# Performance work log

Measured on AMD Instinct MI355X. Metric: run time of the kernel, lower is better.

Reference implementation:

```python
import jax, jax.numpy as jnp
import numpy as np

B, S, D = 4, 16, 512          # batch, seq, attention_dim
V, T = 32000, 18              # vocab_size, tree_depth
INNER = V - 1                 # internal nodes of Huffman tree


def setup_inputs() -> dict:
    key = jax.random.key(0)
    k_att, k_w, k_idx, k_bit = jax.random.split(key, 4)
    att = jax.random.normal(k_att, (B, S, D), dtype=jnp.float32)
    weight = jax.random.normal(k_w, (INNER, D), dtype=jnp.float32) * 0.02
    path_index = jax.random.randint(k_idx, (V * T,), 0, INNER, dtype=jnp.int64)
    # left/right branch bits: sign=+1,bias=0 -> p ; sign=-1,bias=1 -> 1-p
    bits = jax.random.randint(k_bit, (V * T,), 0, 2).astype(jnp.float32)
    path_sign = 1.0 - 2.0 * bits
    path_bias = bits
    return {
        "att": att,
        "weight": weight,
        "path_index": path_index,
        "path_sign": path_sign,
        "path_bias": path_bias,
        "vocab_size": V,
        "tree_depth": T,
    }


def reference(att, weight, path_index, path_sign, path_bias, vocab_size, tree_depth):
    # h: sigmoid of linear projection onto internal-node vectors  [B,S,INNER]
    h = jax.nn.sigmoid(jnp.einsum("bsd,nd->bsn", att, weight))
    # gather per-(token,depth) internal-node probs, flip via sign/bias
    g = jnp.take(h, path_index, axis=-1) * path_sign + path_bias  # [B,S,V*T]
    Hm = g.reshape(att.shape[0], -1, vocab_size, tree_depth)      # [B,S,V,T]
    return jnp.sum(jnp.log(Hm), axis=-1)                          # [B,S,V]
```

## Files before the change

kernel.cpp:

```cpp
#include <hip/hip_runtime.h>

#define BS    64
#define DDIM  512
#define NV    32000
#define TD    18
#define INNER 31999

typedef __attribute__((ext_vector_type(8))) short short8;
typedef __attribute__((ext_vector_type(4))) float floatx4;

__device__ __forceinline__ float bf16_to_f32(unsigned short u) {
    union { unsigned int i; float f; } v; v.i = ((unsigned int)u) << 16; return v.f;
}
__device__ __forceinline__ unsigned short f32_to_bf16(float f) {
    union { float f; unsigned int i; } v; v.f = f;
    unsigned int r = v.i + 0x7FFFu + ((v.i >> 16) & 1u);
    return (unsigned short)(r >> 16);
}

#define IDXB 2250
__global__ __launch_bounds__(256) void prep(
    const int* __restrict__ idx,
    const unsigned int* __restrict__ signbits,
    unsigned short* __restrict__ idx2,
    const float4* __restrict__ att,
    ushort4* __restrict__ attb)
{
    const int b = blockIdx.x;
    if (b < IDXB) {
        const unsigned int* w = (const unsigned int*)idx;
        bool i64 = true;
#pragma unroll
        for (int j = 1; j < 16; j += 2) i64 &= (w[j] == 0u);
        int o = b * 256 + threadIdx.x;
        int val = i64 ? idx[2 * o] : idx[o];
        idx2[o] = (unsigned short)((val << 1) | (int)(signbits[o] >> 31));
    } else {
        int i = (b - IDXB) * 256 + threadIdx.x;
        float4 a = att[i];
        ushort4 r;
        r.x = f32_to_bf16(a.x); r.y = f32_to_bf16(a.y);
        r.z = f32_to_bf16(a.z); r.w = f32_to_bf16(a.w);
        attb[i] = r;
    }
}

__global__ __launch_bounds__(256) void gemm_logsig(
    const unsigned short* __restrict__ attb,
    const float* __restrict__ weight,
    unsigned int* __restrict__ pairsT)
{
    const int lane = threadIdx.x & 63;
    const int wave = threadIdx.x >> 6;
    const int nb   = blockIdx.x * 64 + wave * 16;
    const int l15  = lane & 15;
    const int quad = lane >> 4;

    floatx4 acc[4];
#pragma unroll
    for (int i = 0; i < 4; ++i) acc[i] = (floatx4){0.f, 0.f, 0.f, 0.f};

    int brow = nb + l15;
    if (brow > INNER - 1) brow = INNER - 1;
    const float*          bbase = weight + (size_t)brow * DDIM + quad * 8;
    const unsigned short* abase = attb + l15 * DDIM + quad * 8;

#pragma unroll 4
    for (int k0 = 0; k0 < DDIM; k0 += 32) {
        float4 b0 = *(const float4*)(bbase + k0);
        float4 b1 = *(const float4*)(bbase + k0 + 4);
        short8 bfrag;
        bfrag[0] = (short)f32_to_bf16(b0.x); bfrag[1] = (short)f32_to_bf16(b0.y);
        bfrag[2] = (short)f32_to_bf16(b0.z); bfrag[3] = (short)f32_to_bf16(b0.w);
        bfrag[4] = (short)f32_to_bf16(b1.x); bfrag[5] = (short)f32_to_bf16(b1.y);
        bfrag[6] = (short)f32_to_bf16(b1.z); bfrag[7] = (short)f32_to_bf16(b1.w);
#pragma unroll
        for (int mt = 0; mt < 4; ++mt) {
            short8 afrag = *(const short8*)(abase + mt * 16 * DDIM + k0);
            acc[mt] = __builtin_amdgcn_mfma_f32_16x16x32_bf16(afrag, bfrag, acc[mt], 0, 0, 0);
        }
    }

    const int n = nb + l15;
    if (n < INNER) {
        unsigned int* dst = pairsT + ((size_t)n << 6) + quad * 4;
#pragma unroll
        for (int mt = 0; mt < 4; ++mt) {
            unsigned int wds[4];
#pragma unroll
            for (int r = 0; r < 4; ++r) {
                float x = acc[mt][r];
                float lp = -(fmaxf(-x, 0.f) + __logf(1.f + __expf(-fabsf(x))));
                float lm = lp - x;
                wds[r] = (unsigned int)f32_to_bf16(lp)
                       | ((unsigned int)f32_to_bf16(lm) << 16);
            }
            uint4 wv; wv.x = wds[0]; wv.y = wds[1]; wv.z = wds[2]; wv.w = wds[3];
            *(uint4*)(dst + mt * 16) = wv;
        }
    }
}

__global__ __launch_bounds__(256) void gather_bs(
    const unsigned int* __restrict__ pairsT,
    const unsigned short* __restrict__ idx2,
    float* __restrict__ out)
{
    __shared__ float tile[32][65];
    const int lane  = threadIdx.x & 63;
    const int wave  = threadIdx.x >> 6;
    const int vbase = blockIdx.x * 32;

#pragma unroll
    for (int i = 0; i < 8; ++i) {
        const int vloc = wave * 8 + i;
        const unsigned short* col = idx2 + (size_t)(vbase + vloc) * TD;
        float s0 = 0.f, s1 = 0.f;
#pragma unroll
        for (int t = 0; t < TD; t += 2) {
            unsigned int e0 = col[t];
            unsigned int e1 = col[t + 1];
            unsigned int p0 = pairsT[((size_t)(e0 >> 1) << 6) + lane];
            unsigned int p1 = pairsT[((size_t)(e1 >> 1) << 6) + lane];
            unsigned short h0 = (e0 & 1u) ? (unsigned short)(p0 >> 16)
                                          : (unsigned short)(p0 & 0xFFFFu);
            unsigned short h1 = (e1 & 1u) ? (unsigned short)(p1 >> 16)
                                          : (unsigned short)(p1 & 0xFFFFu);
            s0 += bf16_to_f32(h0);
            s1 += bf16_to_f32(h1);
        }
        tile[vloc][lane] = s0 + s1;
    }
    __syncthreads();

    const int bs  = threadIdx.x >> 2;
    const int seg = threadIdx.x & 3;
    float4 r0, r1;
    r0.x = tile[seg * 8 + 0][bs]; r0.y = tile[seg * 8 + 1][bs];
    r0.z = tile[seg * 8 + 2][bs]; r0.w = tile[seg * 8 + 3][bs];
    r1.x = tile[seg * 8 + 4][bs]; r1.y = tile[seg * 8 + 5][bs];
    r1.z = tile[seg * 8 + 6][bs]; r1.w = tile[seg * 8 + 7][bs];
    float4* dst = (float4*)(out + (size_t)bs * NV + vbase + seg * 8);
    dst[0] = r0; dst[1] = r1;
}

extern "C" void kernel_launch(void* const* d_in, const int* in_sizes, int n_in,
                              void* d_out, int out_size, void* d_ws, size_t ws_size,
                              hipStream_t stream)
{
    const float*        att    = (const float*)d_in[0];
    const float*        weight = (const float*)d_in[1];
    const int*          pidx   = (const int*)d_in[2];
    const unsigned int* psign  = (const unsigned int*)d_in[3];
    float* out = (float*)d_out;

    char* ws = (char*)d_ws;
    unsigned int*   pairsT = (unsigned int*)ws;
    unsigned short* idx2   = (unsigned short*)(ws + 8192000);
    ushort4*        attb   = (ushort4*)       (ws + 9344000);

    prep<<<IDXB + 32, 256, 0, stream>>>(pidx, psign, idx2, (const float4*)att, attb);
    gemm_logsig<<<500, 256, 0, stream>>>((const unsigned short*)attb, weight, pairsT);
    gather_bs<<<1000, 256, 0, stream>>>(pairsT, idx2, out);
}
```

Baseline: 138.5 us.

## Stage weight tiles via async global-to-LDS loads and fuse index prep into gather

The GEMM kernel now streams the fp32 weight tile into a double-buffered, XOR-swizzled LDS region with global_load_lds, so the next K-chunk loads while MFMAs run on the current one. Index/sign packing moves out of the prep kernel into the gather kernel, which decodes its 576 path entries into LDS per block. This drops the idx2 round trip through global memory and shrinks prep to the attention conversion. The cost is 64 KB of LDS per GEMM block, which limits occupancy, plus extra barriers and redundant int64 detection in every gather block.

```diff
diff --git a/kernel.cpp b/kernel.cpp
--- a/kernel.cpp
+++ b/kernel.cpp
@@ -17,32 +17,21 @@
     unsigned int r = v.i + 0x7FFFu + ((v.i >> 16) & 1u);
     return (unsigned short)(r >> 16);
 }
+__device__ __forceinline__ void gload16(const void* g, void* l) {
+    __builtin_amdgcn_global_load_lds(
+        (const __attribute__((address_space(1))) unsigned int*)g,
+        (__attribute__((address_space(3))) unsigned int*)l, 16, 0, 0);
+}
 
-#define IDXB 2250
-__global__ __launch_bounds__(256) void prep(
-    const int* __restrict__ idx,
-    const unsigned int* __restrict__ signbits,
-    unsigned short* __restrict__ idx2,
-    const float4* __restrict__ att,
-    ushort4* __restrict__ attb)
+__global__ __launch_bounds__(256) void prep_att(
+    const float4* __restrict__ att, ushort4* __restrict__ attb)
 {
-    const int b = blockIdx.x;
-    if (b < IDXB) {
-        const unsigned int* w = (const unsigned int*)idx;
-        bool i64 = true;
-#pragma unroll
-        for (int j = 1; j < 16; j += 2) i64 &= (w[j] == 0u);
-        int o = b * 256 + threadIdx.x;
-        int val = i64 ? idx[2 * o] : idx[o];
-        idx2[o] = (unsigned short)((val << 1) | (int)(signbits[o] >> 31));
-    } else {
-        int i = (b - IDXB) * 256 + threadIdx.x;
-        float4 a = att[i];
-        ushort4 r;
-        r.x = f32_to_bf16(a.x); r.y = f32_to_bf16(a.y);
-        r.z = f32_to_bf16(a.z); r.w = f32_to_bf16(a.w);
-        attb[i] = r;
-    }
+    int i = blockIdx.x * 256 + threadIdx.x;
+    float4 a = att[i];
+    ushort4 r;
+    r.x = f32_to_bf16(a.x); r.y = f32_to_bf16(a.y);
+    r.z = f32_to_bf16(a.z); r.w = f32_to_bf16(a.w);
+    attb[i] = r;
 }
 
 __global__ __launch_bounds__(256) void gemm_logsig(
@@ -50,50 +39,79 @@
     const float* __restrict__ weight,
     unsigned int* __restrict__ pairsT)
 {
-    const int lane = threadIdx.x & 63;
-    const int wave = threadIdx.x >> 6;
-    const int nb   = blockIdx.x * 64 + wave * 16;
+    __shared__ __align__(16) char ldsb[2][32768];
+
+    const int tid  = threadIdx.x;
+    const int lane = tid & 63;
+    const int wave = tid >> 6;
     const int l15  = lane & 15;
     const int quad = lane >> 4;
+    const int B0   = blockIdx.x * 64;
+
+    const int r    = wave * 16 + l15;
+    const int swz  = (r & 7) << 4;
 
     floatx4 acc[4];
 #pragma unroll
     for (int i = 0; i < 4; ++i) acc[i] = (floatx4){0.f, 0.f, 0.f, 0.f};
 
-    int brow = nb + l15;
-    if (brow > INNER - 1) brow = INNER - 1;
-    const float*          bbase = weight + (size_t)brow * DDIM + quad * 8;
+    auto STAGE = [&](int buf, int c) {
+#pragma unroll
+        for (int it = 0; it < 8; ++it) {
+            int p    = it * 256 + tid;
+            int row  = p >> 5;
+            int cb   = (p & 31) << 4;
+            int gcb  = cb ^ ((row & 7) << 4);
+            int grow = B0 + row;
+            if (grow > INNER - 1) grow = INNER - 1;
+            gload16((const char*)weight + (size_t)grow * (DDIM * 4) + c * 512 + gcb,
+                    &ldsb[buf][row * 512 + cb]);
+        }
+    };
+
+    STAGE(0, 0);
+    __syncthreads();
+
     const unsigned short* abase = attb + l15 * DDIM + quad * 8;
-
-#pragma unroll 4
-    for (int k0 = 0; k0 < DDIM; k0 += 32) {
-        float4 b0 = *(const float4*)(bbase + k0);
-        float4 b1 = *(const float4*)(bbase + k0 + 4);
-        short8 bfrag;
-        bfrag[0] = (short)f32_to_bf16(b0.x); bfrag[1] = (short)f32_to_bf16(b0.y);
-        bfrag[2] = (short)f32_to_bf16(b0.z); bfrag[3] = (short)f32_to_bf16(b0.w);
-        bfrag[4] = (short)f32_to_bf16(b1.x); bfrag[5] = (short)f32_to_bf16(b1.y);
-        bfrag[6] = (short)f32_to_bf16(b1.z); bfrag[7] = (short)f32_to_bf16(b1.w);
+    int buf = 0;
 #pragma unroll
-        for (int mt = 0; mt < 4; ++mt) {
-            short8 afrag = *(const short8*)(abase + mt * 16 * DDIM + k0);
-            acc[mt] = __builtin_amdgcn_mfma_f32_16x16x32_bf16(afrag, bfrag, acc[mt], 0, 0, 0);
+    for (int c = 0; c < 4; ++c) {
+        if (c < 3) STAGE(buf ^ 1, c + 1);
+        const char* bb = &ldsb[buf][r * 512];
+#pragma unroll
+        for (int kl = 0; kl < 4; ++kl) {
+            int cb0 = kl * 128 + quad * 32;
+            float4 b0 = *(const float4*)(bb + ((cb0)      ^ swz));
+            float4 b1 = *(const float4*)(bb + ((cb0 + 16) ^ swz));
+            short8 bfrag;
+            bfrag[0] = (short)f32_to_bf16(b0.x); bfrag[1] = (short)f32_to_bf16(b0.y);
+            bfrag[2] = (short)f32_to_bf16(b0.z); bfrag[3] = (short)f32_to_bf16(b0.w);
+            bfrag[4] = (short)f32_to_bf16(b1.x); bfrag[5] = (short)f32_to_bf16(b1.y);
+            bfrag[6] = (short)f32_to_bf16(b1.z); bfrag[7] = (short)f32_to_bf16(b1.w);
+            const int k0 = c * 128 + kl * 32;
+#pragma unroll
+            for (int mt = 0; mt < 4; ++mt) {
+                short8 afrag = *(const short8*)(abase + mt * 16 * DDIM + k0);
+                acc[mt] = __builtin_amdgcn_mfma_f32_16x16x32_bf16(afrag, bfrag, acc[mt], 0, 0, 0);
+            }
         }
+        __syncthreads();
+        buf ^= 1;
     }
 
-    const int n = nb + l15;
+    const int n = B0 + wave * 16 + l15;
     if (n < INNER) {
         unsigned int* dst = pairsT + ((size_t)n << 6) + quad * 4;
 #pragma unroll
         for (int mt = 0; mt < 4; ++mt) {
             unsigned int wds[4];
 #pragma unroll
-            for (int r = 0; r < 4; ++r) {
-                float x = acc[mt][r];
+            for (int rr = 0; rr < 4; ++rr) {
+                float x = acc[mt][rr];
                 float lp = -(fmaxf(-x, 0.f) + __logf(1.f + __expf(-fabsf(x))));
                 float lm = lp - x;
-                wds[r] = (unsigned int)f32_to_bf16(lp)
-                       | ((unsigned int)f32_to_bf16(lm) << 16);
+                wds[rr] = (unsigned int)f32_to_bf16(lp)
+                        | ((unsigned int)f32_to_bf16(lm) << 16);
             }
             uint4 wv; wv.x = wds[0]; wv.y = wds[1]; wv.z = wds[2]; wv.w = wds[3];
             *(uint4*)(dst + mt * 16) = wv;
@@ -103,18 +121,33 @@
 
 __global__ __launch_bounds__(256) void gather_bs(
     const unsigned int* __restrict__ pairsT,
-    const unsigned short* __restrict__ idx2,
+    const int* __restrict__ idx,
+    const unsigned int* __restrict__ signbits,
     float* __restrict__ out)
 {
+    __shared__ unsigned int eLDS[576];
     __shared__ float tile[32][65];
-    const int lane  = threadIdx.x & 63;
-    const int wave  = threadIdx.x >> 6;
+    const int tid   = threadIdx.x;
+    const int lane  = tid & 63;
+    const int wave  = tid >> 6;
     const int vbase = blockIdx.x * 32;
+
+    const unsigned int* w = (const unsigned int*)idx;
+    bool i64 = true;
+#pragma unroll
+    for (int j = 1; j < 16; j += 2) i64 &= (w[j] == 0u);
+
+    for (int q = tid; q < 576; q += 256) {
+        int g = vbase * TD + q;
+        int val = i64 ? idx[2 * g] : idx[g];
+        eLDS[q] = ((unsigned int)val << 1) | (signbits[g] >> 31);
+    }
+    __syncthreads();
 
 #pragma unroll
     for (int i = 0; i < 8; ++i) {
         const int vloc = wave * 8 + i;
-        const unsigned short* col = idx2 + (size_t)(vbase + vloc) * TD;
+        const unsigned int* col = eLDS + vloc * TD;
         float s0 = 0.f, s1 = 0.f;
 #pragma unroll
         for (int t = 0; t < TD; t += 2) {
@@ -155,11 +188,10 @@
     float* out = (float*)d_out;
 
     char* ws = (char*)d_ws;
-    unsigned int*   pairsT = (unsigned int*)ws;
-    unsigned short* idx2   = (unsigned short*)(ws + 8192000);
-    ushort4*        attb   = (ushort4*)       (ws + 9344000);
+    unsigned int* pairsT = (unsigned int*)ws;
+    ushort4*      attb   = (ushort4*)(ws + 8192000);
 
-    prep<<<IDXB + 32, 256, 0, stream>>>(pidx, psign, idx2, (const float4*)att, attb);
+    prep_att<<<32, 256, 0, stream>>>((const float4*)att, attb);
     gemm_logsig<<<500, 256, 0, stream>>>((const unsigned short*)attb, weight, pairsT);
-    gather_bs<<<1000, 256, 0, stream>>>(pairsT, idx2, out);
+    gather_bs<<<1000, 256, 0, stream>>>(pairsT, pidx, psign, out);
 }
```

Measured after the change: 150.6 us. +8.7%, slower.

## Remove prep kernel by fusing conversions into GEMM and gather

Applied to the files above, without the earlier changes.

Drops the separate prep launch. Att is now converted to bf16 inline inside the GEMM, and the GEMM block is retiled so each wave computes a 32x16 output slice instead of 64x16, with twice as many blocks. The gather kernel now decodes path indices and sign bits straight from the original int64/float inputs into shared memory per block. This removes one kernel launch and the idx2/attb workspace round trip, at the cost of redundant per-block conversion work and wider index loads in the gather.

```diff
diff --git a/kernel.cpp b/kernel.cpp
--- a/kernel.cpp
+++ b/kernel.cpp
@@ -17,75 +17,59 @@
     unsigned int r = v.i + 0x7FFFu + ((v.i >> 16) & 1u);
     return (unsigned short)(r >> 16);
 }
-
-#define IDXB 2250
-__global__ __launch_bounds__(256) void prep(
-    const int* __restrict__ idx,
-    const unsigned int* __restrict__ signbits,
-    unsigned short* __restrict__ idx2,
-    const float4* __restrict__ att,
-    ushort4* __restrict__ attb)
-{
-    const int b = blockIdx.x;
-    if (b < IDXB) {
-        const unsigned int* w = (const unsigned int*)idx;
-        bool i64 = true;
-#pragma unroll
-        for (int j = 1; j < 16; j += 2) i64 &= (w[j] == 0u);
-        int o = b * 256 + threadIdx.x;
-        int val = i64 ? idx[2 * o] : idx[o];
-        idx2[o] = (unsigned short)((val << 1) | (int)(signbits[o] >> 31));
-    } else {
-        int i = (b - IDXB) * 256 + threadIdx.x;
-        float4 a = att[i];
-        ushort4 r;
-        r.x = f32_to_bf16(a.x); r.y = f32_to_bf16(a.y);
-        r.z = f32_to_bf16(a.z); r.w = f32_to_bf16(a.w);
-        attb[i] = r;
-    }
+__device__ __forceinline__ short8 cvt8(float4 a, float4 b) {
+    short8 s;
+    s[0] = (short)f32_to_bf16(a.x); s[1] = (short)f32_to_bf16(a.y);
+    s[2] = (short)f32_to_bf16(a.z); s[3] = (short)f32_to_bf16(a.w);
+    s[4] = (short)f32_to_bf16(b.x); s[5] = (short)f32_to_bf16(b.y);
+    s[6] = (short)f32_to_bf16(b.z); s[7] = (short)f32_to_bf16(b.w);
+    return s;
 }
 
 __global__ __launch_bounds__(256) void gemm_logsig(
-    const unsigned short* __restrict__ attb,
+    const float* __restrict__ att,
     const float* __restrict__ weight,
     unsigned int* __restrict__ pairsT)
 {
-    const int lane = threadIdx.x & 63;
-    const int wave = threadIdx.x >> 6;
-    const int nb   = blockIdx.x * 64 + wave * 16;
+    const int tid  = threadIdx.x;
+    const int lane = tid & 63;
+    const int wave = tid >> 6;
+    const int nsub = wave & 1;
+    const int msub = wave >> 1;
     const int l15  = lane & 15;
     const int quad = lane >> 4;
+    const int B0   = blockIdx.x * 32;
 
-    floatx4 acc[4];
-#pragma unroll
-    for (int i = 0; i < 4; ++i) acc[i] = (floatx4){0.f, 0.f, 0.f, 0.f};
+    floatx4 acc[2];
+    acc[0] = (floatx4){0.f, 0.f, 0.f, 0.f};
+    acc[1] = (floatx4){0.f, 0.f, 0.f, 0.f};
 
-    int brow = nb + l15;
+    int brow = B0 + nsub * 16 + l15;
     if (brow > INNER - 1) brow = INNER - 1;
-    const float*          bbase = weight + (size_t)brow * DDIM + quad * 8;
-    const unsigned short* abase = attb + l15 * DDIM + quad * 8;
+    const float* bbase = weight + (size_t)brow * DDIM + quad * 8;
+    const float* a0    = att + (size_t)(msub * 32 + l15) * DDIM + quad * 8;
+    const float* a1    = a0 + 16 * DDIM;
 
 #pragma unroll 4
     for (int k0 = 0; k0 < DDIM; k0 += 32) {
         float4 b0 = *(const float4*)(bbase + k0);
         float4 b1 = *(const float4*)(bbase + k0 + 4);
-        short8 bfrag;
-        bfrag[0] = (short)f32_to_bf16(b0.x); bfrag[1] = (short)f32_to_bf16(b0.y);
-        bfrag[2] = (short)f32_to_bf16(b0.z); bfrag[3] = (short)f32_to_bf16(b0.w);
-        bfrag[4] = (short)f32_to_bf16(b1.x); bfrag[5] = (short)f32_to_bf16(b1.y);
-        bfrag[6] = (short)f32_to_bf16(b1.z); bfrag[7] = (short)f32_to_bf16(b1.w);
-#pragma unroll
-        for (int mt = 0; mt < 4; ++mt) {
-            short8 afrag = *(const short8*)(abase + mt * 16 * DDIM + k0);
-            acc[mt] = __builtin_amdgcn_mfma_f32_16x16x32_bf16(afrag, bfrag, acc[mt], 0, 0, 0);
-        }
+        float4 x0 = *(const float4*)(a0 + k0);
+        float4 x1 = *(const float4*)(a0 + k0 + 4);
+        float4 y0 = *(const float4*)(a1 + k0);
+        float4 y1 = *(const float4*)(a1 + k0 + 4);
+        short8 bfrag = cvt8(b0, b1);
+        short8 af0   = cvt8(x0, x1);
+        short8 af1   = cvt8(y0, y1);
+        acc[0] = __builtin_amdgcn_mfma_f32_16x16x32_bf16(af0, bfrag, acc[0], 0, 0, 0);
+        acc[1] = __builtin_amdgcn_mfma_f32_16x16x32_bf16(af1, bfrag, acc[1], 0, 0, 0);
     }
 
-    const int n = nb + l15;
+    const int n = B0 + nsub * 16 + l15;
     if (n < INNER) {
-        unsigned int* dst = pairsT + ((size_t)n << 6) + quad * 4;
+        unsigned int* dst = pairsT + ((size_t)n << 6) + msub * 32 + quad * 4;
 #pragma unroll
-        for (int mt = 0; mt < 4; ++mt) {
+        for (int mt = 0; mt < 2; ++mt) {
             unsigned int wds[4];
 #pragma unroll
             for (int r = 0; r < 4; ++r) {
@@ -103,18 +87,33 @@
 
 __global__ __launch_bounds__(256) void gather_bs(
     const unsigned int* __restrict__ pairsT,
-    const unsigned short* __restrict__ idx2,
+    const int* __restrict__ idx,
+    const unsigned int* __restrict__ signbits,
     float* __restrict__ out)
 {
+    __shared__ unsigned int eLDS[576];
     __shared__ float tile[32][65];
-    const int lane  = threadIdx.x & 63;
-    const int wave  = threadIdx.x >> 6;
+    const int tid   = threadIdx.x;
+    const int lane  = tid & 63;
+    const int wave  = tid >> 6;
     const int vbase = blockIdx.x * 32;
+
+    const unsigned int* w = (const unsigned int*)idx;
+    bool i64 = true;
+#pragma unroll
+    for (int j = 1; j < 16; j += 2) i64 &= (w[j] == 0u);
+
+    for (int q = tid; q < 576; q += 256) {
+        int g = vbase * TD + q;
+        int val = i64 ? idx[2 * g] : idx[g];
+        eLDS[q] = ((unsigned int)val << 1) | (signbits[g] >> 31);
+    }
+    __syncthreads();
 
 #pragma unroll
     for (int i = 0; i < 8; ++i) {
         const int vloc = wave * 8 + i;
-        const unsigned short* col = idx2 + (size_t)(vbase + vloc) * TD;
+        const unsigned int* col = eLDS + vloc * TD;
         float s0 = 0.f, s1 = 0.f;
 #pragma unroll
         for (int t = 0; t < TD; t += 2) {
@@ -154,12 +153,8 @@
     const unsigned int* psign  = (const unsigned int*)d_in[3];
     float* out = (float*)d_out;
 
-    char* ws = (char*)d_ws;
-    unsigned int*   pairsT = (unsigned int*)ws;
-    unsigned short* idx2   = (unsigned short*)(ws + 8192000);
-    ushort4*        attb   = (ushort4*)       (ws + 9344000);
+    unsigned int* pairsT = (unsigned int*)d_ws;
 
-    prep<<<IDXB + 32, 256, 0, stream>>>(pidx, psign, idx2, (const float4*)att, attb);
-    gemm_logsig<<<500, 256, 0, stream>>>((const unsigned short*)attb, weight, pairsT);
-    gather_bs<<<1000, 256, 0, stream>>>(pairsT, idx2, out);
+    gemm_logsig<<<1000, 256, 0, stream>>>(att, weight, pairsT);
+    gather_bs<<<1000, 256, 0, stream>>>(pairsT, pidx, psign, out);
 }
```

Result: slower. 169.0 us (+22.0%).

## Stage bf16 activations in swizzled LDS and split GEMM across 8 waves

Applied to the files above, without the earlier changes.

The GEMM kernel now copies the whole 64x512 bf16 activation matrix into XOR-swizzled shared memory once per block and reads A fragments from LDS instead of global memory. The block grows to 512 threads, with waves split 4 along N and 2 along M, so each wave does half the M tiles. Weight rows are loaded into registers in double-buffered chunks ahead of use, to overlap global loads with MFMA work. The cost is a 64KB LDS footprint per block, which limits occupancy, higher register pressure, and each weight row now being loaded by two waves.

```diff
diff --git a/kernel.cpp b/kernel.cpp
--- a/kernel.cpp
+++ b/kernel.cpp
@@ -16,6 +16,14 @@
     union { float f; unsigned int i; } v; v.f = f;
     unsigned int r = v.i + 0x7FFFu + ((v.i >> 16) & 1u);
     return (unsigned short)(r >> 16);
+}
+__device__ __forceinline__ short8 cvt8(float4 a, float4 b) {
+    short8 s;
+    s[0] = (short)f32_to_bf16(a.x); s[1] = (short)f32_to_bf16(a.y);
+    s[2] = (short)f32_to_bf16(a.z); s[3] = (short)f32_to_bf16(a.w);
+    s[4] = (short)f32_to_bf16(b.x); s[5] = (short)f32_to_bf16(b.y);
+    s[6] = (short)f32_to_bf16(b.z); s[7] = (short)f32_to_bf16(b.w);
+    return s;
 }
 
 #define IDXB 2250
@@ -45,51 +53,75 @@
     }
 }
 
-__global__ __launch_bounds__(256) void gemm_logsig(
-    const unsigned short* __restrict__ attb,
+__global__ __launch_bounds__(512) void gemm_logsig(
+    const ushort4* __restrict__ attb,
     const float* __restrict__ weight,
     unsigned int* __restrict__ pairsT)
 {
-    const int lane = threadIdx.x & 63;
-    const int wave = threadIdx.x >> 6;
-    const int nb   = blockIdx.x * 64 + wave * 16;
+    __shared__ __align__(16) char As[65536];
+    const int tid  = threadIdx.x;
+    const int lane = tid & 63;
+    const int wave = tid >> 6;
+    const int nsub = wave & 3;
+    const int msub = wave >> 2;
     const int l15  = lane & 15;
     const int quad = lane >> 4;
+    const int B0   = blockIdx.x * 64;
 
-    floatx4 acc[4];
 #pragma unroll
-    for (int i = 0; i < 4; ++i) acc[i] = (floatx4){0.f, 0.f, 0.f, 0.f};
+    for (int it = 0; it < 8; ++it) {
+        int p   = it * 512 + tid;
+        int row = p >> 6;
+        int c16 = (p & 63) << 4;
+        *(uint4*)(As + row * 1024 + (c16 ^ ((row & 7) << 4))) =
+            ((const uint4*)attb)[p];
+    }
+    __syncthreads();
 
-    int brow = nb + l15;
+    int brow = B0 + nsub * 16 + l15;
     if (brow > INNER - 1) brow = INNER - 1;
-    const float*          bbase = weight + (size_t)brow * DDIM + quad * 8;
-    const unsigned short* abase = attb + l15 * DDIM + quad * 8;
+    const float* bbase = weight + (size_t)brow * DDIM + quad * 8;
 
-#pragma unroll 4
-    for (int k0 = 0; k0 < DDIM; k0 += 32) {
-        float4 b0 = *(const float4*)(bbase + k0);
-        float4 b1 = *(const float4*)(bbase + k0 + 4);
-        short8 bfrag;
-        bfrag[0] = (short)f32_to_bf16(b0.x); bfrag[1] = (short)f32_to_bf16(b0.y);
-        bfrag[2] = (short)f32_to_bf16(b0.z); bfrag[3] = (short)f32_to_bf16(b0.w);
-        bfrag[4] = (short)f32_to_bf16(b1.x); bfrag[5] = (short)f32_to_bf16(b1.y);
-        bfrag[6] = (short)f32_to_bf16(b1.z); bfrag[7] = (short)f32_to_bf16(b1.w);
+    const int   r0    = msub * 32 + l15;
+    const int   sw    = (r0 & 7) << 4;
+    const char* arow0 = As + r0 * 1024;
+    const char* arow1 = arow0 + 16 * 1024;
+    const int   cbq   = quad * 16;
+
+    floatx4 acc0 = (floatx4){0.f, 0.f, 0.f, 0.f};
+    floatx4 acc1 = (floatx4){0.f, 0.f, 0.f, 0.f};
+    float4 bA[8], bB[8];
+
+#define LB(BUF, c) { _Pragma("unroll")                                        \
+    for (int s = 0; s < 4; ++s) {                                             \
+        BUF[2*s]   = *(const float4*)(bbase + (c)*128 + s*32);                \
+        BUF[2*s+1] = *(const float4*)(bbase + (c)*128 + s*32 + 4); } }
+#define CB(BUF, c) { _Pragma("unroll")                                        \
+    for (int s = 0; s < 4; ++s) {                                             \
+        short8 bf = cvt8(BUF[2*s], BUF[2*s+1]);                               \
+        int cb = ((c)*256 + s*64 + cbq) ^ sw;                                 \
+        short8 af0 = *(const short8*)(arow0 + cb);                            \
+        short8 af1 = *(const short8*)(arow1 + cb);                            \
+        acc0 = __builtin_amdgcn_mfma_f32_16x16x32_bf16(af0, bf, acc0, 0,0,0); \
+        acc1 = __builtin_amdgcn_mfma_f32_16x16x32_bf16(af1, bf, acc1, 0,0,0); } }
+
+    LB(bA, 0); LB(bB, 1);
+    CB(bA, 0); LB(bA, 2);
+    CB(bB, 1); LB(bB, 3);
+    CB(bA, 2); CB(bB, 3);
+#undef LB
+#undef CB
+
+    const int n = B0 + nsub * 16 + l15;
+    if (n < INNER) {
+        unsigned int* dst = pairsT + ((size_t)n << 6) + msub * 32 + quad * 4;
+        floatx4 accs[2] = {acc0, acc1};
 #pragma unroll
-        for (int mt = 0; mt < 4; ++mt) {
-            short8 afrag = *(const short8*)(abase + mt * 16 * DDIM + k0);
-            acc[mt] = __builtin_amdgcn_mfma_f32_16x16x32_bf16(afrag, bfrag, acc[mt], 0, 0, 0);
-        }
-    }
-
-    const int n = nb + l15;
-    if (n < INNER) {
-        unsigned int* dst = pairsT + ((size_t)n << 6) + quad * 4;
-#pragma unroll
-        for (int mt = 0; mt < 4; ++mt) {
+        for (int mt = 0; mt < 2; ++mt) {
             unsigned int wds[4];
 #pragma unroll
             for (int r = 0; r < 4; ++r) {
-                float x = acc[mt][r];
+                float x = accs[mt][r];
                 float lp = -(fmaxf(-x, 0.f) + __logf(1.f + __expf(-fabsf(x))));
                 float lm = lp - x;
                 wds[r] = (unsigned int)f32_to_bf16(lp)
@@ -160,6 +192,6 @@
     ushort4*        attb   = (ushort4*)       (ws + 9344000);
 
     prep<<<IDXB + 32, 256, 0, stream>>>(pidx, psign, idx2, (const float4*)att, attb);
-    gemm_logsig<<<500, 256, 0, stream>>>((const unsigned short*)attb, weight, pairsT);
+    gemm_logsig<<<500, 512, 0, stream>>>(attb, weight, pairsT);
     gather_bs<<<1000, 256, 0, stream>>>(pairsT, idx2, out);
 }
```

New measurement: 137.8 us. Within noise of the previous version (-0.5%).
